# Kernel optimization log

Hardware: AMD Instinct MI355X
Metric: run time of the kernel (lower is better)

## Reference

```python
import jax, jax.numpy as jnp
import numpy as np

B, NQ, NK, C, OUT = 4, 2048, 2048, 4, 64
H = 16          # hidden size of the radial MLP (hardcoded in MlpRBF)
WINDOW = 0.25   # window_size default in MlpRBF


def setup_inputs() -> dict:
    key = jax.random.key(0)
    ks = jax.random.split(key, 20)
    s = 0.5
    return {
        "key_pos": jax.random.uniform(ks[0], (B, NK, 1), dtype=jnp.float32),
        "queries": jax.random.uniform(ks[1], (B, NQ, 1), dtype=jnp.float32),
        "values": jax.random.normal(ks[2], (B, NK, 1), dtype=jnp.float32),
        "key_chan": jax.random.randint(ks[3], (B, NK), 0, C),
        # radial MLP: 1 -> 16 -> 16 -> 16 -> 1, ReLU hidden activations
        "w0": jax.random.normal(ks[4], (H, 1)) * s, "b0": jax.random.normal(ks[5], (H,)) * 0.1,
        "w1": jax.random.normal(ks[6], (H, H)) * (s / np.sqrt(H)), "b1": jax.random.normal(ks[7], (H,)) * 0.1,
        "w2": jax.random.normal(ks[8], (H, H)) * (s / np.sqrt(H)), "b2": jax.random.normal(ks[9], (H,)) * 0.1,
        "w3": jax.random.normal(ks[10], (1, H)) * (s / np.sqrt(H)), "b3": jax.random.normal(ks[11], (1,)) * 0.1,
        # density_transform: Linear(1,1)
        "wd": jax.random.normal(ks[12], (1, 1)) * s, "bd": jax.random.normal(ks[13], (1,)) * 0.1,
        # resizer: Linear(2*C, OUT)
        "wr": jax.random.normal(ks[14], (OUT, 2 * C)) * (s / np.sqrt(2 * C)), "br": jax.random.normal(ks[15], (OUT,)) * 0.1,
    }


def reference(key_pos, queries, values, key_chan,
              w0, b0, w1, b1, w2, b2, w3, b3, wd, bd, wr, br):
    # pairwise |key - query| distances: [B, NQ, NK] (is_abs_dist=True)
    diff = jnp.abs(key_pos[:, None, :, 0] - queries[:, :, None, 0])
    window = diff < WINDOW                              # [B, NQ, NK] bool

    # per-pair radial MLP (x_dim=1 input, 3 hidden layers of 16, scalar out)
    x = diff[..., None]                                 # [B, NQ, NK, 1]
    h = jax.nn.relu(x @ w0.T + b0)
    h = jax.nn.relu(h @ w1.T + b1)
    h = jax.nn.relu(h @ w2.T + b2)
    raw = (h @ w3.T + b3)[..., 0]                       # [B, NQ, NK]
    weight = jnp.abs(raw) * window.astype(raw.dtype)    # mask_and_apply + abs + window mask

    # per-channel masked reduction (equivalent to gathering keys of each channel)
    onehot = jax.nn.one_hot(key_chan, C, dtype=weight.dtype)      # [B, NK, C]
    density = jnp.einsum('bqk,bkc->bqc', weight, onehot)          # [B, NQ, C]
    numer = jnp.einsum('bqk,bkc->bqc', weight, onehot * values)   # values: [B, NK, 1]
    targets = numer / (density + 1e-5)                            # normalized weighted sum

    # density channel: sigmoid(Linear(density*0.1 - 1))
    dens_feat = jax.nn.sigmoid((density * 0.1 - 1.0) * wd[0, 0] + bd[0])

    # per-channel SetConv output is cat([target, density]) -> interleave: [t0,d0,t1,d1,...]
    feat = jnp.stack([targets, dens_feat], axis=-1).reshape(targets.shape[0], targets.shape[1], 2 * C)
    return feat @ wr.T + br                             # [B, NQ, OUT]
```

## Files before the change

kernel.cpp:

```cpp
#include <hip/hip_runtime.h>
#include <math.h>

constexpr int B_  = 4;
constexpr int NQ_ = 2048;
constexpr int NK_ = 2048;
constexpr int C_  = 4;
constexpr int OUT_ = 64;
constexpr int H_  = 16;
constexpr float WINDOW_ = 0.25f;

constexpr int   TAB_   = 4096;
constexpr float SCALE_ = TAB_ / WINDOW_;
constexpr int   QT_    = 8;

__global__ void build_tab(
    const float* __restrict__ w0, const float* __restrict__ b0,
    const float* __restrict__ w1, const float* __restrict__ b1,
    const float* __restrict__ w2, const float* __restrict__ b2,
    const float* __restrict__ w3, const float* __restrict__ b3,
    float2* __restrict__ tab)
{
    const int i = blockIdx.x * blockDim.x + threadIdx.x;
    if (i >= TAB_) return;

    float f[2];
    #pragma unroll
    for (int e = 0; e < 2; ++e) {
        const float x = (float)(i + e) * (1.0f / SCALE_);
        float h[H_], g[H_];
        #pragma unroll
        for (int j = 0; j < H_; ++j)
            h[j] = fmaxf(fmaf(x, w0[j], b0[j]), 0.f);
        #pragma unroll
        for (int j = 0; j < H_; ++j) {
            float a = b1[j];
            #pragma unroll
            for (int k = 0; k < H_; ++k) a = fmaf(w1[j * H_ + k], h[k], a);
            g[j] = fmaxf(a, 0.f);
        }
        #pragma unroll
        for (int j = 0; j < H_; ++j) {
            float a = b2[j];
            #pragma unroll
            for (int k = 0; k < H_; ++k) a = fmaf(w2[j * H_ + k], g[k], a);
            h[j] = fmaxf(a, 0.f);
        }
        float a = b3[0];
        #pragma unroll
        for (int k = 0; k < H_; ++k) a = fmaf(w3[k], h[k], a);
        f[e] = a;
    }
    const float s = (f[1] - f[0]) * SCALE_;
    const float a = fmaf(-s, (float)i * (1.0f / SCALE_), f[0]);
    tab[i] = make_float2(a, s);
}

__global__ __launch_bounds__(256) void setconv_main(
    const float* __restrict__ key_pos,
    const float* __restrict__ queries,
    const float* __restrict__ values,
    const int*   __restrict__ key_chan,
    const float2* __restrict__ tab,
    const float* __restrict__ wd, const float* __restrict__ bd,
    const float* __restrict__ wr, const float* __restrict__ br,
    float* __restrict__ out)
{
    __shared__ __align__(16) float2 ltab[TAB_];

    const int tid = threadIdx.x;

    {
        const float4* t4 = (const float4*)tab;
        float4*       l4 = (float4*)ltab;
        #pragma unroll
        for (int i = 0; i < TAB_ / 2 / 256; ++i)
            l4[i * 256 + tid] = t4[i * 256 + tid];
    }
    __syncthreads();

    const int blk  = blockIdx.x;
    const int b    = blk >> 8;
    const int tile = blk & 255;
    const int wave = tid >> 6;
    const int lane = tid & 63;

    const float* kpb = key_pos  + b * NK_;
    const float* vb  = values   + b * NK_;
    const int*   cb  = key_chan + b * NK_;

    const float wd0 = wd[0];
    const float bd0 = bd[0];

    float wrow[8];
    #pragma unroll
    for (int j = 0; j < 8; ++j) wrow[j] = wr[lane * 8 + j];
    const float brv = br[lane];

    #pragma unroll
    for (int qq = 0; qq < 2; ++qq) {
        const int   qi   = tile * QT_ + wave * 2 + qq;
        const float qpos = queries[b * NQ_ + qi];

        float d0 = 0.f, d1 = 0.f, d2 = 0.f, d3 = 0.f;
        float n0 = 0.f, n1 = 0.f, n2 = 0.f, n3 = 0.f;

        #pragma unroll 4
        for (int it = 0; it < NK_ / 64; ++it) {
            const int   k  = it * 64 + lane;
            const float dd = fabsf(kpb[k] - qpos);
            const float t  = fminf(dd * SCALE_, (float)(TAB_ - 1));
            const int   ci = (int)t;
            const float2 as = ltab[ci];
            const float raw = fabsf(fmaf(as.y, dd, as.x));
            const float w   = (dd < WINDOW_) ? raw : 0.f;
            const float wv  = w * vb[k];
            const int   ch  = cb[k];
            const float m0 = (ch == 0) ? 1.f : 0.f;
            const float m1 = (ch == 1) ? 1.f : 0.f;
            const float m2 = (ch == 2) ? 1.f : 0.f;
            const float m3 = (ch == 3) ? 1.f : 0.f;
            d0 = fmaf(m0, w, d0);  n0 = fmaf(m0, wv, n0);
            d1 = fmaf(m1, w, d1);  n1 = fmaf(m1, wv, n1);
            d2 = fmaf(m2, w, d2);  n2 = fmaf(m2, wv, n2);
            d3 = fmaf(m3, w, d3);  n3 = fmaf(m3, wv, n3);
        }

        #pragma unroll
        for (int off = 32; off >= 1; off >>= 1) {
            d0 += __shfl_xor(d0, off, 64);  n0 += __shfl_xor(n0, off, 64);
            d1 += __shfl_xor(d1, off, 64);  n1 += __shfl_xor(n1, off, 64);
            d2 += __shfl_xor(d2, off, 64);  n2 += __shfl_xor(n2, off, 64);
            d3 += __shfl_xor(d3, off, 64);  n3 += __shfl_xor(n3, off, 64);
        }

        const float dens[4] = {d0, d1, d2, d3};
        const float num [4] = {n0, n1, n2, n3};

        float acc = brv;
        #pragma unroll
        for (int c = 0; c < 4; ++c) {
            const float tgt = num[c] / (dens[c] + 1e-5f);
            const float x   = (dens[c] * 0.1f - 1.0f) * wd0 + bd0;
            const float df  = 1.0f / (1.0f + expf(-x));
            acc = fmaf(wrow[2 * c],     tgt, acc);
            acc = fmaf(wrow[2 * c + 1], df,  acc);
        }
        out[(b * NQ_ + qi) * OUT_ + lane] = acc;
    }
}

extern "C" void kernel_launch(void* const* d_in, const int* in_sizes, int n_in,
                              void* d_out, int out_size, void* d_ws, size_t ws_size,
                              hipStream_t stream) {
    (void)in_sizes; (void)n_in; (void)out_size; (void)ws_size;

    float2* tab = (float2*)d_ws;

    build_tab<<<dim3((TAB_ + 255) / 256), dim3(256), 0, stream>>>(
        (const float*)d_in[4],  (const float*)d_in[5],
        (const float*)d_in[6],  (const float*)d_in[7],
        (const float*)d_in[8],  (const float*)d_in[9],
        (const float*)d_in[10], (const float*)d_in[11],
        tab);

    setconv_main<<<dim3(B_ * (NQ_ / QT_)), dim3(256), 0, stream>>>(
        (const float*)d_in[0],
        (const float*)d_in[1],
        (const float*)d_in[2],
        (const int*)  d_in[3],
        tab,
        (const float*)d_in[12], (const float*)d_in[13],
        (const float*)d_in[14], (const float*)d_in[15],
        (float*)d_out);
}
```

Measured before the change: 108.6 us.

## Sort keys per channel and scan only the query's window

New measurement: 129.2 us. 1.19x slower.

```diff
diff --git a/kernel.cpp b/kernel.cpp
--- a/kernel.cpp
+++ b/kernel.cpp
@@ -12,57 +12,129 @@
 constexpr int   TAB_   = 4096;
 constexpr float SCALE_ = TAB_ / WINDOW_;
 constexpr int   QT_    = 8;
-
-__global__ void build_tab(
+constexpr int   SLOT_  = 1024;
+constexpr int   NBIN_  = 64;
+constexpr float SENT_  = 4e9f;
+
+constexpr size_t OFF_TAB  = 0;
+constexpr size_t OFF_SORT = 32768;
+constexpr size_t OFF_BINS = 32768 + 16 * SLOT_ * 8;
+
+__global__ __launch_bounds__(256) void preprocess(
+    const float* __restrict__ key_pos,
+    const float* __restrict__ values,
+    const int*   __restrict__ key_chan,
     const float* __restrict__ w0, const float* __restrict__ b0,
     const float* __restrict__ w1, const float* __restrict__ b1,
     const float* __restrict__ w2, const float* __restrict__ b2,
     const float* __restrict__ w3, const float* __restrict__ b3,
-    float2* __restrict__ tab)
+    float2* __restrict__ tab,
+    float2* __restrict__ sorted,
+    int*    __restrict__ bins)
 {
-    const int i = blockIdx.x * blockDim.x + threadIdx.x;
-    if (i >= TAB_) return;
-
-    float f[2];
-    #pragma unroll
-    for (int e = 0; e < 2; ++e) {
-        const float x = (float)(i + e) * (1.0f / SCALE_);
-        float h[H_], g[H_];
-        #pragma unroll
-        for (int j = 0; j < H_; ++j)
-            h[j] = fmaxf(fmaf(x, w0[j], b0[j]), 0.f);
-        #pragma unroll
-        for (int j = 0; j < H_; ++j) {
-            float a = b1[j];
-            #pragma unroll
-            for (int k = 0; k < H_; ++k) a = fmaf(w1[j * H_ + k], h[k], a);
-            g[j] = fmaxf(a, 0.f);
-        }
-        #pragma unroll
-        for (int j = 0; j < H_; ++j) {
-            float a = b2[j];
-            #pragma unroll
-            for (int k = 0; k < H_; ++k) a = fmaf(w2[j * H_ + k], g[k], a);
-            h[j] = fmaxf(a, 0.f);
-        }
-        float a = b3[0];
-        #pragma unroll
-        for (int k = 0; k < H_; ++k) a = fmaf(w3[k], h[k], a);
-        f[e] = a;
-    }
-    const float s = (f[1] - f[0]) * SCALE_;
-    const float a = fmaf(-s, (float)i * (1.0f / SCALE_), f[0]);
-    tab[i] = make_float2(a, s);
+    const int tid = threadIdx.x;
+
+    if (blockIdx.x < 16) {
+        const int i = blockIdx.x * 256 + tid;
+        float f[2];
+        #pragma unroll
+        for (int e = 0; e < 2; ++e) {
+            const float x = (float)(i + e) * (1.0f / SCALE_);
+            float h[H_], g[H_];
+            #pragma unroll
+            for (int j = 0; j < H_; ++j)
+                h[j] = fmaxf(fmaf(x, w0[j], b0[j]), 0.f);
+            #pragma unroll
+            for (int j = 0; j < H_; ++j) {
+                float a = b1[j];
+                #pragma unroll
+                for (int k = 0; k < H_; ++k) a = fmaf(w1[j * H_ + k], h[k], a);
+                g[j] = fmaxf(a, 0.f);
+            }
+            #pragma unroll
+            for (int j = 0; j < H_; ++j) {
+                float a = b2[j];
+                #pragma unroll
+                for (int k = 0; k < H_; ++k) a = fmaf(w2[j * H_ + k], g[k], a);
+                h[j] = fmaxf(a, 0.f);
+            }
+            float a = b3[0];
+            #pragma unroll
+            for (int k = 0; k < H_; ++k) a = fmaf(w3[k], h[k], a);
+            f[e] = a;
+        }
+        const float s = (f[1] - f[0]) * SCALE_;
+        const float a = fmaf(-s, (float)i * (1.0f / SCALE_), f[0]);
+        tab[i] = make_float2(a, s);
+        return;
+    }
+
+    const int slot = blockIdx.x - 16;
+    const int b    = slot >> 2;
+    const int c    = slot & 3;
+
+    __shared__ float spos[SLOT_];
+    __shared__ float sval[SLOT_];
+    __shared__ int   scnt;
+    if (tid == 0) scnt = 0;
+    __syncthreads();
+
+    for (int i = tid; i < NK_; i += 256) {
+        if (key_chan[b * NK_ + i] == c) {
+            const int idx = atomicAdd(&scnt, 1);
+            if (idx < SLOT_) {
+                spos[idx] = key_pos[b * NK_ + i];
+                sval[idx] = values[b * NK_ + i];
+            }
+        }
+    }
+    __syncthreads();
+    const int cnt = (scnt < SLOT_) ? scnt : SLOT_;
+    for (int i = tid; i < SLOT_; i += 256)
+        if (i >= cnt) { spos[i] = SENT_; sval[i] = 0.f; }
+    __syncthreads();
+
+    for (int k2 = 2; k2 <= SLOT_; k2 <<= 1) {
+        for (int j = k2 >> 1; j > 0; j >>= 1) {
+            #pragma unroll
+            for (int base = 0; base < SLOT_; base += 256) {
+                const int i   = base + tid;
+                const int ixj = i ^ j;
+                if (ixj > i) {
+                    const float pa = spos[i], pb = spos[ixj];
+                    const bool  up = (i & k2) == 0;
+                    if ((pa > pb) == up) {
+                        const float va = sval[i], vb = sval[ixj];
+                        spos[i] = pb; spos[ixj] = pa;
+                        sval[i] = vb; sval[ixj] = va;
+                    }
+                }
+            }
+            __syncthreads();
+        }
+    }
+
+    for (int i = tid; i < SLOT_; i += 256)
+        sorted[slot * SLOT_ + i] = make_float2(spos[i], sval[i]);
+
+    if (tid <= NBIN_) {
+        const float bnd = (float)tid * (1.0f / NBIN_);
+        int lo = 0, hi = SLOT_;
+        while (lo < hi) {
+            const int mid = (lo + hi) >> 1;
+            if (spos[mid] < bnd) lo = mid + 1; else hi = mid;
+        }
+        bins[slot * (NBIN_ + 1) + tid] = lo;
+    }
 }
 
 __global__ __launch_bounds__(256) void setconv_main(
-    const float* __restrict__ key_pos,
-    const float* __restrict__ queries,
-    const float* __restrict__ values,
-    const int*   __restrict__ key_chan,
+    const float*  __restrict__ queries,
+    const float2* __restrict__ sorted,
+    const int*    __restrict__ bins,
     const float2* __restrict__ tab,
-    const float* __restrict__ wd, const float* __restrict__ bd,
-    const float* __restrict__ wr, const float* __restrict__ br,
+    const float*  __restrict__ wd, const float* __restrict__ bd,
+    const float*  __restrict__ wr, const float* __restrict__ br,
     float* __restrict__ out)
 {
     __shared__ __align__(16) float2 ltab[TAB_];
@@ -84,10 +156,6 @@
     const int wave = tid >> 6;
     const int lane = tid & 63;
 
-    const float* kpb = key_pos  + b * NK_;
-    const float* vb  = values   + b * NK_;
-    const int*   cb  = key_chan + b * NK_;
-
     const float wd0 = wd[0];
     const float bd0 = bd[0];
 
@@ -101,40 +169,42 @@
         const int   qi   = tile * QT_ + wave * 2 + qq;
         const float qpos = queries[b * NQ_ + qi];
 
-        float d0 = 0.f, d1 = 0.f, d2 = 0.f, d3 = 0.f;
-        float n0 = 0.f, n1 = 0.f, n2 = 0.f, n3 = 0.f;
-
-        #pragma unroll 4
-        for (int it = 0; it < NK_ / 64; ++it) {
-            const int   k  = it * 64 + lane;
-            const float dd = fabsf(kpb[k] - qpos);
-            const float t  = fminf(dd * SCALE_, (float)(TAB_ - 1));
-            const int   ci = (int)t;
-            const float2 as = ltab[ci];
-            const float raw = fabsf(fmaf(as.y, dd, as.x));
-            const float w   = (dd < WINDOW_) ? raw : 0.f;
-            const float wv  = w * vb[k];
-            const int   ch  = cb[k];
-            const float m0 = (ch == 0) ? 1.f : 0.f;
-            const float m1 = (ch == 1) ? 1.f : 0.f;
-            const float m2 = (ch == 2) ? 1.f : 0.f;
-            const float m3 = (ch == 3) ? 1.f : 0.f;
-            d0 = fmaf(m0, w, d0);  n0 = fmaf(m0, wv, n0);
-            d1 = fmaf(m1, w, d1);  n1 = fmaf(m1, wv, n1);
-            d2 = fmaf(m2, w, d2);  n2 = fmaf(m2, wv, n2);
-            d3 = fmaf(m3, w, d3);  n3 = fmaf(m3, wv, n3);
+        int lo_bin = (int)floorf((qpos - WINDOW_) * (float)NBIN_);
+        lo_bin = (lo_bin < 0) ? 0 : ((lo_bin > NBIN_) ? NBIN_ : lo_bin);
+        int hi_bin = (int)ceilf((qpos + WINDOW_) * (float)NBIN_);
+        hi_bin = (hi_bin < 0) ? 0 : ((hi_bin > NBIN_) ? NBIN_ : hi_bin);
+
+        float dens[4], num[4];
+        #pragma unroll
+        for (int c = 0; c < 4; ++c) {
+            const int slot = b * 4 + c;
+            const int* bs  = bins + slot * (NBIN_ + 1);
+            const int lo = bs[lo_bin] & ~63;
+            const int hi = (bs[hi_bin] + 63) & ~63;
+            const float2* seg = sorted + slot * SLOT_;
+
+            float d = 0.f, n = 0.f;
+            for (int k = lo; k < hi; k += 64) {
+                const float2 pv = seg[k + lane];
+                const float dd  = fabsf(pv.x - qpos);
+                const float t   = fminf(dd * SCALE_, (float)(TAB_ - 1));
+                const float2 as = ltab[(int)t];
+                const float raw = fabsf(fmaf(as.y, dd, as.x));
+                const float w   = (dd < WINDOW_) ? raw : 0.f;
+                d += w;
+                n  = fmaf(w, pv.y, n);
+            }
+            dens[c] = d; num[c] = n;
         }
 
         #pragma unroll
         for (int off = 32; off >= 1; off >>= 1) {
-            d0 += __shfl_xor(d0, off, 64);  n0 += __shfl_xor(n0, off, 64);
-            d1 += __shfl_xor(d1, off, 64);  n1 += __shfl_xor(n1, off, 64);
-            d2 += __shfl_xor(d2, off, 64);  n2 += __shfl_xor(n2, off, 64);
-            d3 += __shfl_xor(d3, off, 64);  n3 += __shfl_xor(n3, off, 64);
-        }
-
-        const float dens[4] = {d0, d1, d2, d3};
-        const float num [4] = {n0, n1, n2, n3};
+            #pragma unroll
+            for (int c = 0; c < 4; ++c) {
+                dens[c] += __shfl_xor(dens[c], off, 64);
+                num [c] += __shfl_xor(num [c], off, 64);
+            }
+        }
 
         float acc = brv;
         #pragma unroll
@@ -154,21 +224,24 @@
                               hipStream_t stream) {
     (void)in_sizes; (void)n_in; (void)out_size; (void)ws_size;
 
-    float2* tab = (float2*)d_ws;
-
-    build_tab<<<dim3((TAB_ + 255) / 256), dim3(256), 0, stream>>>(
+    char* ws = (char*)d_ws;
+    float2* tab    = (float2*)(ws + OFF_TAB);
+    float2* sorted = (float2*)(ws + OFF_SORT);
+    int*    bins   = (int*)   (ws + OFF_BINS);
+
+    preprocess<<<dim3(32), dim3(256), 0, stream>>>(
+        (const float*)d_in[0],
+        (const float*)d_in[2],
+        (const int*)  d_in[3],
         (const float*)d_in[4],  (const float*)d_in[5],
         (const float*)d_in[6],  (const float*)d_in[7],
         (const float*)d_in[8],  (const float*)d_in[9],
         (const float*)d_in[10], (const float*)d_in[11],
-        tab);
+        tab, sorted, bins);
 
     setconv_main<<<dim3(B_ * (NQ_ / QT_)), dim3(256), 0, stream>>>(
-        (const float*)d_in[0],
         (const float*)d_in[1],
-        (const float*)d_in[2],
-        (const int*)  d_in[3],
-        tab,
+        sorted, bins, tab,
         (const float*)d_in[12], (const float*)d_in[13],
         (const float*)d_in[14], (const float*)d_in[15],
         (float*)d_out);
```
